# Kernel optimization log

Hardware: AMD Instinct MI355X
Metric: run time of the kernel (lower is better)

The kernel has to match this reference:

```python
import jax, jax.numpy as jnp
import numpy as np

EPS = 1e-13

def masked_softmax(scores, mask):
    # scores: [B, L1, L2], mask: [B, L2] binary float
    # ESIM-style: softmax(scores * mask) * mask, renormalized.
    m = mask[:, None, :]                      # [B, 1, L2]
    r = jax.nn.softmax(scores * m, axis=-1) * m
    return r / (r.sum(axis=-1, keepdims=True) + EPS)

def weighted_sum(attn, tensor, mask):
    # attn: [B, L1, L2], tensor: [B, L2, D], mask: [B, L1]
    return jnp.matmul(attn, tensor) * mask[:, :, None]

def setup_inputs() -> dict:
    key = jax.random.key(0)
    k1, k2, k3, k4 = jax.random.split(key, 4)
    B, Lp, Lh, D = 64, 512, 512, 600
    encoded_premise = jax.random.normal(k1, (B, Lp, D), dtype=jnp.float32)
    encoded_hypothesis = jax.random.normal(k2, (B, Lh, D), dtype=jnp.float32)
    # binary padding masks (1 = valid token)
    premise_mask = (jax.random.uniform(k3, (B, Lp)) > 0.15).astype(jnp.float32)
    hypothesis_mask = (jax.random.uniform(k4, (B, Lh)) > 0.15).astype(jnp.float32)
    return {"encoded_premise": encoded_premise, "premise_mask": premise_mask,
            "encoded_hypothesis": encoded_hypothesis, "hypothesis_mask": hypothesis_mask}

def reference(encoded_premise, premise_mask, encoded_hypothesis, hypothesis_mask):
    # shared cross-attention score matrix [B, Lp, Lh]
    attn = jnp.einsum('bpd,bhd->bph', encoded_premise, encoded_hypothesis)
    a_p = masked_softmax(attn, hypothesis_mask)                    # [B, Lp, Lh]
    a_h = masked_softmax(attn.transpose(0, 2, 1), premise_mask)    # [B, Lh, Lp]
    weighted_premise = weighted_sum(a_p, encoded_hypothesis, premise_mask)      # [B, Lp, D]
    weighted_hypothesis = weighted_sum(a_h, encoded_premise, hypothesis_mask)   # [B, Lh, D]
    return (weighted_premise, weighted_hypothesis)
```

## Files before the change

### kernel.cpp

```cpp
#include <hip/hip_runtime.h>
#include <hip/hip_bf16.h>

#define DEVB 64
#define LSEQ 512
#define DDIM 600

typedef short short8 __attribute__((ext_vector_type(8)));
typedef float f32x4 __attribute__((ext_vector_type(4)));
typedef _Float16 f16x8 __attribute__((ext_vector_type(8)));
typedef _Float16 f16x4 __attribute__((ext_vector_type(4)));

constexpr int LDP = 40;

__device__ __forceinline__ unsigned short f2bf(float x) {
    union { float f; unsigned u; } v; v.f = x;
    unsigned r = v.u + 0x7fffu + ((v.u >> 16) & 1u);
    return (unsigned short)(r >> 16);
}
__device__ __forceinline__ unsigned pk16(float a, float b) {
    union { _Float16 h[2]; unsigned u; } p;
    p.h[0] = (_Float16)a; p.h[1] = (_Float16)b;
    return p.u;
}
__device__ __forceinline__ f32x4 mfma16(short8 a, short8 b, f32x4 c) {
    return __builtin_amdgcn_mfma_f32_16x16x32_bf16(a, b, c, 0, 0, 0);
}
__device__ __forceinline__ f32x4 mfma16h(f16x8 a, f16x8 b, f32x4 c) {
    return __builtin_amdgcn_mfma_f32_16x16x32_f16(a, b, c, 0, 0, 0);
}

typedef const __attribute__((address_space(1))) unsigned int* as1_u32p;
typedef __attribute__((address_space(3))) unsigned int* as3_u32p;
__device__ __forceinline__ void gll16(const void* g, void* l) {
    __builtin_amdgcn_global_load_lds((as1_u32p)g, (as3_u32p)l, 16, 0, 0);
}

__global__ __launch_bounds__(256) void transcvt3(
    const float* __restrict__ P, const float* __restrict__ H,
    _Float16* __restrict__ pT, _Float16* __restrict__ hT)
{
    int blk = blockIdx.x;
    const float* X; _Float16* XT;
    const int half = DEVB * 40;
    if (blk < half) { X = P; XT = pT; }
    else { blk -= half; X = H; XT = hT; }

    int b   = blk / 40;
    int rem = blk % 40;
    int r0  = (rem / 5) << 6;
    int d0  = (rem % 5) << 7;
    const float* Xb = X + (size_t)b * LSEQ * DDIM;

    __shared__ unsigned T32[2][64 * 33];
    const int t  = threadIdx.x;
    const int rp = t >> 3;
    const int dc = (t & 7) << 3;

#pragma unroll
    for (int ht_ = 0; ht_ < 2; ++ht_) {
        int dd = d0 + (ht_ << 6) + dc;
        if (dd < DDIM) {
            const float* s0 = Xb + (size_t)(r0 + 2 * rp) * DDIM + dd;
            const float* s1 = s0 + DDIM;
            float4 a0 = *(const float4*)s0, a1 = *(const float4*)(s0 + 4);
            float4 b0 = *(const float4*)s1, b1 = *(const float4*)(s1 + 4);
            float xa[8] = {a0.x, a0.y, a0.z, a0.w, a1.x, a1.y, a1.z, a1.w};
            float xb[8] = {b0.x, b0.y, b0.z, b0.w, b1.x, b1.y, b1.z, b1.w};
#pragma unroll
            for (int j = 0; j < 8; ++j)
                T32[ht_][(dc + j) * 33 + rp] = pk16(xa[j], xb[j]);
        }
    }
    __syncthreads();

    const int dl = t >> 2;
    const int q  = t & 3;
#pragma unroll
    for (int ht_ = 0; ht_ < 2; ++ht_) {
        int d = d0 + (ht_ << 6) + dl;
        if (d < DDIM) {
            unsigned buf[8];
#pragma unroll
            for (int i = 0; i < 8; ++i)
                buf[i] = T32[ht_][dl * 33 + q * 8 + i];
            unsigned* dst = (unsigned*)(XT + ((size_t)b * DDIM + d) * LSEQ + r0) + q * 8;
            *(uint4*)(dst)     = *(uint4*)&buf[0];
            *(uint4*)(dst + 4) = *(uint4*)&buf[4];
        }
    }
}

__global__ __launch_bounds__(256) void attn_gemm(
    const float* __restrict__ P, const float* __restrict__ H,
    float* __restrict__ attn)
{
    const int bid = blockIdx.x;
    const int swz = (bid & 7) * 128 + (bid >> 3);
    const int b  = swz >> 4;
    const int pt = ((swz >> 2) & 3) << 7;
    const int ht = (swz & 3) << 7;
    const float* Pb = P + ((size_t)b * LSEQ + pt) * DDIM;
    const float* Hb = H + ((size_t)b * LSEQ + ht) * DDIM;
    float* Ab = attn + (size_t)b * LSEQ * LSEQ;

    __shared__ _Float16 Ah[2][128 * 32], Al[2][128 * 32], Bh[2][128 * 32];

    const int t    = threadIdx.x;
    const int lane = t & 63;
    const int wave = t >> 6;
    const int wm = (wave >> 1) << 6;
    const int wn = (wave & 1) << 6;
    const int fr = lane & 15;
    const int fq = lane >> 4;
    const int srow = t >> 2;
    const int sc8  = (t & 3) << 3;

    const int wchunk = (t & 3) ^ ((srow >> 1) & 3);
    const int woff   = srow * 32 + (wchunk << 3);
    const int rcoff  = ((fq ^ ((fr >> 1) & 3)) << 3);

    float4 pf[8];
    const float4 fz = {0.f, 0.f, 0.f, 0.f};
    auto issue = [&](int k0) {
        bool ok = (k0 + sc8) < DDIM;
#pragma unroll
        for (int r = 0; r < 2; ++r) {
            size_t base = (size_t)(srow + (r << 6)) * DDIM + k0 + sc8;
            if (ok) {
                pf[r * 4 + 0] = *(const float4*)(Pb + base);
                pf[r * 4 + 1] = *(const float4*)(Pb + base + 4);
                pf[r * 4 + 2] = *(const float4*)(Hb + base);
                pf[r * 4 + 3] = *(const float4*)(Hb + base + 4);
            } else {
                pf[r * 4 + 0] = fz; pf[r * 4 + 1] = fz;
                pf[r * 4 + 2] = fz; pf[r * 4 + 3] = fz;
            }
        }
    };
    auto wr = [&](int buf) {
#pragma unroll
        for (int r = 0; r < 2; ++r) {
            float4 a0 = pf[r * 4 + 0], a1 = pf[r * 4 + 1];
            float4 h0 = pf[r * 4 + 2], h1 = pf[r * 4 + 3];
            float af[8] = {a0.x, a0.y, a0.z, a0.w, a1.x, a1.y, a1.z, a1.w};
            float hf[8] = {h0.x, h0.y, h0.z, h0.w, h1.x, h1.y, h1.z, h1.w};
            f16x8 hi, lo, bh;
#pragma unroll
            for (int j = 0; j < 8; ++j) {
                hi[j] = (_Float16)af[j];
                lo[j] = (_Float16)(af[j] - (float)hi[j]);
                bh[j] = (_Float16)hf[j];
            }
            int off = woff + (r << 11);
            *(f16x8*)&Ah[buf][off] = hi;
            *(f16x8*)&Al[buf][off] = lo;
            *(f16x8*)&Bh[buf][off] = bh;
        }
    };

    issue(0);
    wr(0);
    issue(32);
    __syncthreads();

    f32x4 acc[4][4];
#pragma unroll
    for (int i = 0; i < 4; ++i)
#pragma unroll
        for (int j = 0; j < 4; ++j) acc[i][j] = (f32x4){0.f, 0.f, 0.f, 0.f};

    constexpr int NK = 19;
    int cur = 0;
    for (int it = 0; it < NK; ++it) {
        f16x8 ah[4], al[4], bh[4];
#pragma unroll
        for (int i = 0; i < 4; ++i) {
            int ra = (wm + (i << 4) + fr) * 32 + rcoff;
            int rb = (wn + (i << 4) + fr) * 32 + rcoff;
            ah[i] = *(const f16x8*)&Ah[cur][ra];
            al[i] = *(const f16x8*)&Al[cur][ra];
            bh[i] = *(const f16x8*)&Bh[cur][rb];
        }
        if (it + 1 < NK) {
            wr(cur ^ 1);
            if (it + 2 < NK) issue((it + 2) << 5);
        }
#pragma unroll
        for (int mi = 0; mi < 4; ++mi)
#pragma unroll
            for (int ni = 0; ni < 4; ++ni) {
                f32x4 c = acc[mi][ni];
                c = mfma16h(ah[mi], bh[ni], c);
                c = mfma16h(al[mi], bh[ni], c);
                acc[mi][ni] = c;
            }
        __syncthreads();
        cur ^= 1;
    }

#pragma unroll
    for (int mi = 0; mi < 4; ++mi)
#pragma unroll
        for (int ni = 0; ni < 4; ++ni)
#pragma unroll
            for (int j = 0; j < 4; ++j) {
                int p = pt + wm + (mi << 4) + (fq << 2) + j;
                int h = ht + wn + (ni << 4) + fr;
                Ab[(size_t)p * LSEQ + h] = acc[mi][ni][j];
            }
}

__global__ __launch_bounds__(256) void stats_w1(
    const float* __restrict__ attn, const float* __restrict__ hmask,
    const float* __restrict__ pmask,
    float* __restrict__ M1, float* __restrict__ R1,
    _Float16* __restrict__ W1,
    float* __restrict__ Mp, float* __restrict__ Tp, float* __restrict__ Sp)
{
    int b      = blockIdx.x >> 4;
    int stripe = blockIdx.x & 15;
    int lane   = threadIdx.x & 63;
    int wave   = threadIdx.x >> 6;
    const float* hm = hmask + (b << 9);
    const float* pm = pmask + (b << 9);

    float4 m0 = *(const float4*)(hm + (lane << 3));
    float4 m1 = *(const float4*)(hm + (lane << 3) + 4);
    float mk[8] = {m0.x, m0.y, m0.z, m0.w, m1.x, m1.y, m1.z, m1.w};

    float cM[8], cT[8], cS[8];
#pragma unroll
    for (int j = 0; j < 8; ++j) { cM[j] = -1e30f; cT[j] = 0.f; cS[j] = 0.f; }

    for (int i = 0; i < 8; ++i) {
        int row   = (stripe << 5) + (wave << 3) + i;
        int rowid = (b << 9) + row;
        const float* rp = attn + (size_t)rowid * LSEQ + (lane << 3);
        float4 s0 = *(const float4*)rp;
        float4 s1 = *(const float4*)(rp + 4);
        float s[8] = {s0.x, s0.y, s0.z, s0.w, s1.x, s1.y, s1.z, s1.w};

        float v[8];
#pragma unroll
        for (int j = 0; j < 8; ++j) v[j] = s[j] * mk[j];
        float mx = -1e30f;
#pragma unroll
        for (int j = 0; j < 8; ++j) mx = fmaxf(mx, v[j]);
#pragma unroll
        for (int off = 32; off; off >>= 1) mx = fmaxf(mx, __shfl_xor(mx, off));

        float e[8], T = 0.f, S = 0.f;
#pragma unroll
        for (int j = 0; j < 8; ++j) { e[j] = __expf(v[j] - mx); T += mk[j] * e[j]; S += e[j]; }
#pragma unroll
        for (int off = 32; off; off >>= 1) { T += __shfl_xor(T, off); S += __shfl_xor(S, off); }
        float R = 1.f / (T + 1e-13f * S);

        if (W1) {
            union { f16x8 v8; _Float16 h[8]; } wv;
#pragma unroll
            for (int j = 0; j < 8; ++j) wv.h[j] = (_Float16)(mk[j] * e[j] * R);
            *(f16x8*)(W1 + (size_t)rowid * LSEQ + (lane << 3)) = wv.v8;
        } else if (lane == 0) {
            M1[rowid] = mx; R1[rowid] = R;
        }

        float pmv = pm[row];
#pragma unroll
        for (int j = 0; j < 8; ++j) {
            float v2 = s[j] * pmv;
            float nm = fmaxf(cM[j], v2);
            float sc = __expf(cM[j] - nm);
            float e2 = __expf(v2 - nm);
            cT[j] = cT[j] * sc + pmv * e2;
            cS[j] = cS[j] * sc + e2;
            cM[j] = nm;
        }
    }

    __shared__ float LM[4][512], LT[4][512], LS[4][512];
#pragma unroll
    for (int j = 0; j < 8; ++j) {
        int c = (lane << 3) + j;
        LM[wave][c] = cM[j]; LT[wave][c] = cT[j]; LS[wave][c] = cS[j];
    }
    __syncthreads();

    size_t base = (size_t)((b << 4) + stripe) * 512;
    for (int cc = threadIdx.x; cc < 512; cc += 256) {
        float gm = fmaxf(fmaxf(LM[0][cc], LM[1][cc]), fmaxf(LM[2][cc], LM[3][cc]));
        float gT = 0.f, gS = 0.f;
#pragma unroll
        for (int w = 0; w < 4; ++w) {
            float sc = __expf(LM[w][cc] - gm);
            gT += LT[w][cc] * sc;
            gS += LS[w][cc] * sc;
        }
        Mp[base + cc] = gm; Tp[base + cc] = gT; Sp[base + cc] = gS;
    }
}

__global__ __launch_bounds__(256) void col_merge(
    const float* __restrict__ Mp, const float* __restrict__ Tp,
    const float* __restrict__ Sp, float* __restrict__ M2, float* __restrict__ R2)
{
    int b = blockIdx.x >> 1;
    int c = ((blockIdx.x & 1) << 8) + threadIdx.x;
    float gm = -1e30f, gT = 0.f, gS = 0.f;
#pragma unroll
    for (int st = 0; st < 16; ++st) {
        size_t idx = (size_t)((b << 4) + st) * 512 + c;
        float m = Mp[idx], tt = Tp[idx], ss = Sp[idx];
        float nm  = fmaxf(gm, m);
        float sc1 = __expf(gm - nm), sc2 = __expf(m - nm);
        gT = gT * sc1 + tt * sc2;
        gS = gS * sc1 + ss * sc2;
        gm = nm;
    }
    M2[(b << 9) + c] = gm;
    R2[(b << 9) + c] = 1.f / (gT + 1e-13f * gS);
}

__global__ __launch_bounds__(256) void w2gen3(
    const float* __restrict__ attn, const float* __restrict__ pmask,
    const float* __restrict__ Mp, const float* __restrict__ Tp,
    const float* __restrict__ Sp, _Float16* __restrict__ W2)
{
    int blk = blockIdx.x;
    int b  = blk >> 5;
    int p0 = ((blk >> 2) & 7) << 6;
    int h0 = (blk & 3) << 7;
    const float* Ab = attn + (size_t)b * LSEQ * LSEQ;
    const float* pm = pmask + (b << 9);

    __shared__ float sM[128], sR[128];
    __shared__ unsigned T32[128 * 33];
    const int t = threadIdx.x;
    if (t < 128) {
        float gm = -1e30f, gT = 0.f, gS = 0.f;
#pragma unroll
        for (int st = 0; st < 16; ++st) {
            size_t idx = (size_t)((b << 4) + st) * 512 + h0 + t;
            float m = Mp[idx], tt = Tp[idx], ss = Sp[idx];
            float nm  = fmaxf(gm, m);
            float sc1 = __expf(gm - nm), sc2 = __expf(m - nm);
            gT = gT * sc1 + tt * sc2;
            gS = gS * sc1 + ss * sc2;
            gm = nm;
        }
        sM[t] = gm;
        sR[t] = 1.f / (gT + 1e-13f * gS);
    }
    __syncthreads();

#pragma unroll
    for (int it = 0; it < 4; ++it) {
        int g  = t + (it << 8);
        int pp = g >> 5;
        int hc = (g & 31) << 2;
        const float* s0 = Ab + (size_t)(p0 + 2 * pp) * LSEQ + h0 + hc;
        float4 xa = *(const float4*)s0;
        float4 xb = *(const float4*)(s0 + LSEQ);
        float pa = pm[p0 + 2 * pp];
        float pb = pm[p0 + 2 * pp + 1];
        float a[4] = {xa.x, xa.y, xa.z, xa.w};
        float bb[4] = {xb.x, xb.y, xb.z, xb.w};
#pragma unroll
        for (int j = 0; j < 4; ++j) {
            float wa = (pa != 0.f) ? __expf(a[j]  - sM[hc + j]) * sR[hc + j] : 0.f;
            float wb = (pb != 0.f) ? __expf(bb[j] - sM[hc + j]) * sR[hc + j] : 0.f;
            T32[(hc + j) * 33 + pp] = pk16(wa, wb);
        }
    }
    __syncthreads();

    const int hl = t >> 1;
    const int q  = t & 1;
    unsigned buf[16];
#pragma unroll
    for (int i = 0; i < 16; ++i)
        buf[i] = T32[hl * 33 + q * 16 + i];
    unsigned* dst = (unsigned*)(W2 + ((size_t)(b << 9) + h0 + hl) * LSEQ + p0) + q * 16;
#pragma unroll
    for (int i = 0; i < 4; ++i)
        *(uint4*)(dst + 4 * i) = *(uint4*)&buf[4 * i];
}

__global__ __launch_bounds__(256) void gemm_gll(
    const _Float16* __restrict__ W, const _Float16* __restrict__ BT,
    const float* __restrict__ mask_m, float* __restrict__ out)
{
    const int bid = blockIdx.x;
    const int swz = (bid & 7) * 160 + (bid >> 3);
    const int b   = swz / 20;
    const int rem = swz % 20;
    const int m0  = (rem / 5) << 7;
    const int n0  = (rem % 5) << 7;
    const _Float16* Wb = W  + (size_t)b * LSEQ * LSEQ;
    const _Float16* Bb = BT + (size_t)b * DDIM * LSEQ;

    __shared__ _Float16 Wl[2][128 * 32];
    __shared__ _Float16 Bl[2][128 * 32];

    const int t    = threadIdx.x;
    const int lane = t & 63;
    const int wave = t >> 6;
    const int wm = (wave >> 1) << 6;
    const int wn = (wave & 1) << 6;
    const int fr = lane & 15;
    const int fq = lane >> 4;
    const int rcoff = ((fq ^ ((fr >> 1) & 3)) << 3);

    const int rowc0 = (wave << 5) + (lane >> 2);
    auto stage = [&](int buf, int k0) {
#pragma unroll
        for (int c = 0; c < 2; ++c) {
            int row = rowc0 + (c << 4);
            int lg  = (((lane & 3) ^ ((row >> 1) & 3)) << 3);
            int ldsoff = ((wave << 5) + (c << 4)) * 32;
            gll16(Wb + (size_t)(m0 + row) * LSEQ + k0 + lg, &Wl[buf][ldsoff]);
            gll16(Bb + (size_t)(n0 + row) * LSEQ + k0 + lg, &Bl[buf][ldsoff]);
        }
    };

    stage(0, 0);
    __syncthreads();

    f32x4 acc[4][4];
#pragma unroll
    for (int i = 0; i < 4; ++i)
#pragma unroll
        for (int j = 0; j < 4; ++j) acc[i][j] = (f32x4){0.f, 0.f, 0.f, 0.f};

    constexpr int NK = 16;
    for (int it = 0; it < NK; ++it) {
        int cur = it & 1;
        if (it + 1 < NK) stage(cur ^ 1, (it + 1) << 5);

        f16x8 af[4], bfr[4];
#pragma unroll
        for (int i = 0; i < 4; ++i) {
            af[i]  = *(const f16x8*)&Wl[cur][(wm + (i << 4) + fr) * 32 + rcoff];
            bfr[i] = *(const f16x8*)&Bl[cur][(wn + (i << 4) + fr) * 32 + rcoff];
        }
#pragma unroll
        for (int mi = 0; mi < 4; ++mi)
#pragma unroll
            for (int ni = 0; ni < 4; ++ni)
                acc[mi][ni] = mfma16h(af[mi], bfr[ni], acc[mi][ni]);
        __syncthreads();
    }

    const float* mmb = mask_m + (b << 9) + m0;
#pragma unroll
    for (int mi = 0; mi < 4; ++mi)
#pragma unroll
        for (int j = 0; j < 4; ++j) {
            int row = wm + (mi << 4) + (fq << 2) + j;
            float mm = mmb[row];
#pragma unroll
            for (int ni = 0; ni < 4; ++ni) {
                int d = n0 + wn + (ni << 4) + fr;
                if (d < DDIM)
                    out[((size_t)(b << 9) + m0 + row) * DDIM + d] = mm * acc[mi][ni][j];
            }
        }
}

template <int TRANSA>
__global__ __launch_bounds__(256) void wsum(
    const float* __restrict__ attn, const float* __restrict__ Bsrc,
    const float* __restrict__ mask_k, const float* __restrict__ mask_m,
    const float* __restrict__ Mst, const float* __restrict__ Rst,
    float* __restrict__ out)
{
    const int blk = blockIdx.x;
    const int b   = blk / 20;
    const int rem = blk % 20;
    const int m0  = (rem / 5) << 7;
    const int n0  = (rem % 5) << 7;

    const float* Ab  = attn + (size_t)b * LSEQ * LSEQ;
    const float* Bb  = Bsrc + (size_t)b * LSEQ * DDIM;
    const float* mkb = mask_k + (b << 9);

    __shared__ unsigned short Wl[128 * LDP];
    __shared__ unsigned short Bl[128 * LDP];
    __shared__ float Ml[128], Rl[128], Mm[128];

    const int t    = threadIdx.x;
    const int lane = t & 63;
    const int wave = t >> 6;
    const int wm = (wave >> 1) << 6;
    const int wn = (wave & 1) << 6;
    const int fr = lane & 15;
    const int fq = lane >> 4;

    if (t < 128) {
        Ml[t] = Mst[(b << 9) + m0 + t];
        Rl[t] = Rst[(b << 9) + m0 + t];
        Mm[t] = mask_m[(b << 9) + m0 + t];
    }
    __syncthreads();

    f32x4 acc[4][4];
#pragma unroll
    for (int i = 0; i < 4; ++i)
#pragma unroll
        for (int j = 0; j < 4; ++j) acc[i][j] = (f32x4){0.f, 0.f, 0.f, 0.f};

    for (int k0 = 0; k0 < LSEQ; k0 += 32) {
        if constexpr (TRANSA == 0) {
#pragma unroll
            for (int r = 0; r < 4; ++r) {
                int idx = t + (r << 8);
                int row = idx >> 3;
                int c4  = (idx & 7) << 2;
                float4 x  = *(const float4*)(Ab + (size_t)(m0 + row) * LSEQ + k0 + c4);
                float4 km = *(const float4*)(mkb + k0 + c4);
                float Mv = Ml[row], Rv = Rl[row];
                ushort4 w;
                w.x = (km.x != 0.f) ? f2bf(__expf(x.x - Mv) * Rv) : (unsigned short)0;
                w.y = (km.y != 0.f) ? f2bf(__expf(x.y - Mv) * Rv) : (unsigned short)0;
                w.z = (km.z != 0.f) ? f2bf(__expf(x.z - Mv) * Rv) : (unsigned short)0;
                w.w = (km.w != 0.f) ? f2bf(__expf(x.w - Mv) * Rv) : (unsigned short)0;
                *(ushort4*)&Wl[row * LDP + c4] = w;
            }
        } else {
#pragma unroll
            for (int r = 0; r < 4; ++r) {
                int mh = t & 127;
                int pq = (t >> 7) + (r << 1);
                float Mv = Ml[mh], Rv = Rl[mh];
                ushort4 w;
#pragma unroll
                for (int j = 0; j < 4; ++j) {
                    int k = k0 + (pq << 2) + j;
                    float x  = Ab[(size_t)k * LSEQ + m0 + mh];
                    float km = mkb[k];
                    ((unsigned short*)&w)[j] =
                        (km != 0.f) ? f2bf(__expf(x - Mv) * Rv) : (unsigned short)0;
                }
                *(ushort4*)&Wl[mh * LDP + (pq << 2)] = w;
            }
        }
#pragma unroll
        for (int r = 0; r < 4; ++r) {
            int d  = t & 127;
            int kq = (t >> 7) + (r << 1);
            bool valid = (n0 + d) < DDIM;
            ushort4 v;
#pragma unroll
            for (int j = 0; j < 4; ++j) {
                int k = k0 + (kq << 2) + j;
                float x = valid ? Bb[(size_t)k * DDIM + n0 + d] : 0.f;
                ((unsigned short*)&v)[j] = f2bf(x);
            }
            *(ushort4*)&Bl[d * LDP + (kq << 2)] = v;
        }
        __syncthreads();

        short8 af[4], bfr[4];
#pragma unroll
        for (int i = 0; i < 4; ++i) {
            af[i]  = *(const short8*)&Wl[(wm + (i << 4) + fr) * LDP + (fq << 3)];
            bfr[i] = *(const short8*)&Bl[(wn + (i << 4) + fr) * LDP + (fq << 3)];
        }
#pragma unroll
        for (int mi = 0; mi < 4; ++mi)
#pragma unroll
            for (int ni = 0; ni < 4; ++ni)
                acc[mi][ni] = mfma16(af[mi], bfr[ni], acc[mi][ni]);
        __syncthreads();
    }

#pragma unroll
    for (int mi = 0; mi < 4; ++mi)
#pragma unroll
        for (int j = 0; j < 4; ++j) {
            int row = wm + (mi << 4) + (fq << 2) + j;
            float mm = Mm[row];
#pragma unroll
            for (int ni = 0; ni < 4; ++ni) {
                int d = n0 + wn + (ni << 4) + fr;
                if (d < DDIM)
                    out[((size_t)(b << 9) + m0 + row) * DDIM + d] = mm * acc[mi][ni][j];
            }
        }
}

extern "C" void kernel_launch(void* const* d_in, const int* in_sizes, int n_in,
                              void* d_out, int out_size, void* d_ws, size_t ws_size,
                              hipStream_t stream)
{
    const float* P  = (const float*)d_in[0];
    const float* pm = (const float*)d_in[1];
    const float* H  = (const float*)d_in[2];
    const float* hm = (const float*)d_in[3];
    float* out = (float*)d_out;
    char* o  = (char*)d_out;
    char* ws = (char*)d_ws;

    const size_t E = (size_t)DEVB * LSEQ * DDIM;

    _Float16* hT = (_Float16*)(o + 78643200);
    _Float16* W1 = (_Float16*)(o + 117964800);

    const size_t fast_need = 146276352;

    if (ws_size >= fast_need) {
        float*     attn = (float*)ws;
        _Float16*  pT   = (_Float16*)(ws + 67108864);
        _Float16*  W2   = (_Float16*)(ws + 67108864 + 39321600);
        float*     Mp   = (float*)(ws + 139984896);
        float*     Tp   = Mp + (size_t)DEVB * 16 * 512;
        float*     Sp   = Tp + (size_t)DEVB * 16 * 512;

        transcvt3<<<DEVB * 80, 256, 0, stream>>>(P, H, pT, hT);
        attn_gemm<<<DEVB * 16, 256, 0, stream>>>(P, H, attn);
        stats_w1<<<DEVB * 16, 256, 0, stream>>>(attn, hm, pm, nullptr, nullptr,
                                                W1, Mp, Tp, Sp);
        w2gen3<<<DEVB * 32, 256, 0, stream>>>(attn, pm, Mp, Tp, Sp, W2);
        gemm_gll<<<DEVB * 20, 256, 0, stream>>>(W1, hT, pm, out);
        gemm_gll<<<DEVB * 20, 256, 0, stream>>>(W2, pT, hm, out + E);
    } else {
        float* attn = (float*)ws;
        float* Mp   = (float*)(ws + 67108864);
        float* Tp   = Mp + (size_t)DEVB * 16 * 512;
        float* Sp   = Tp + (size_t)DEVB * 16 * 512;
        float* M1   = Sp + (size_t)DEVB * 16 * 512;
        float* R1   = M1 + DEVB * LSEQ;
        float* M2   = R1 + DEVB * LSEQ;
        float* R2   = M2 + DEVB * LSEQ;

        attn_gemm<<<DEVB * 16, 256, 0, stream>>>(P, H, attn);
        stats_w1<<<DEVB * 16, 256, 0, stream>>>(attn, hm, pm, M1, R1, nullptr,
                                                Mp, Tp, Sp);
        col_merge<<<DEVB * 2, 256, 0, stream>>>(Mp, Tp, Sp, M2, R2);
        wsum<0><<<DEVB * 20, 256, 0, stream>>>(attn, H, hm, pm, M1, R1, out);
        wsum<1><<<DEVB * 20, 256, 0, stream>>>(attn, P, pm, hm, M2, R2, out + E);
    }
}
```

Baseline: 301.3 us.

## Precompute padded fp16 H in transpose kernel and stage it via global_load_lds

The transpose/convert kernel now also writes a row-major fp16 copy of H with K padded to 608 into scratch space in the output buffer. The attention GEMM reads this half-size copy and loads its B tile directly into LDS with global_load_lds, instead of loading fp32 H through registers and converting it. This cuts the GEMM's global read traffic for H and its conversion work, at the cost of an extra fp16 write in the prepass. The fallback path now runs the prepass just to produce this copy.

```diff
diff --git a/kernel.cpp b/kernel.cpp
--- a/kernel.cpp
+++ b/kernel.cpp
@@ -4,6 +4,7 @@
 #define DEVB 64
 #define LSEQ 512
 #define DDIM 600
+#define KPAD 608
 
 typedef short short8 __attribute__((ext_vector_type(8)));
 typedef float f32x4 __attribute__((ext_vector_type(4)));
@@ -37,13 +38,14 @@
 
 __global__ __launch_bounds__(256) void transcvt3(
     const float* __restrict__ P, const float* __restrict__ H,
-    _Float16* __restrict__ pT, _Float16* __restrict__ hT)
+    _Float16* __restrict__ pT, _Float16* __restrict__ hT,
+    _Float16* __restrict__ Hhi)
 {
     int blk = blockIdx.x;
-    const float* X; _Float16* XT;
+    const float* X; _Float16* XT; _Float16* RM;
     const int half = DEVB * 40;
-    if (blk < half) { X = P; XT = pT; }
-    else { blk -= half; X = H; XT = hT; }
+    if (blk < half) { X = P; XT = pT; RM = nullptr; }
+    else { blk -= half; X = H; XT = hT; RM = Hhi; }
 
     int b   = blk / 40;
     int rem = blk % 40;
@@ -69,29 +71,46 @@
 #pragma unroll
             for (int j = 0; j < 8; ++j)
                 T32[ht_][(dc + j) * 33 + rp] = pk16(xa[j], xb[j]);
-        }
+            if (RM) {
+                f16x8 ha, hb;
+#pragma unroll
+                for (int j = 0; j < 8; ++j) {
+                    ha[j] = (_Float16)xa[j];
+                    hb[j] = (_Float16)xb[j];
+                }
+                _Float16* rm0 = RM + ((size_t)b * LSEQ + r0 + 2 * rp) * KPAD + dd;
+                *(f16x8*)rm0          = ha;
+                *(f16x8*)(rm0 + KPAD) = hb;
+            }
+        }
+    }
+    if (RM && d0 == 512 && t < 64) {
+        const f16x8 z = {0, 0, 0, 0, 0, 0, 0, 0};
+        *(f16x8*)(RM + ((size_t)b * LSEQ + r0 + t) * KPAD + DDIM) = z;
     }
     __syncthreads();
 
-    const int dl = t >> 2;
-    const int q  = t & 3;
-#pragma unroll
-    for (int ht_ = 0; ht_ < 2; ++ht_) {
-        int d = d0 + (ht_ << 6) + dl;
-        if (d < DDIM) {
-            unsigned buf[8];
-#pragma unroll
-            for (int i = 0; i < 8; ++i)
-                buf[i] = T32[ht_][dl * 33 + q * 8 + i];
-            unsigned* dst = (unsigned*)(XT + ((size_t)b * DDIM + d) * LSEQ + r0) + q * 8;
-            *(uint4*)(dst)     = *(uint4*)&buf[0];
-            *(uint4*)(dst + 4) = *(uint4*)&buf[4];
+    if (XT) {
+        const int dl = t >> 2;
+        const int q  = t & 3;
+#pragma unroll
+        for (int ht_ = 0; ht_ < 2; ++ht_) {
+            int d = d0 + (ht_ << 6) + dl;
+            if (d < DDIM) {
+                unsigned buf[8];
+#pragma unroll
+                for (int i = 0; i < 8; ++i)
+                    buf[i] = T32[ht_][dl * 33 + q * 8 + i];
+                unsigned* dst = (unsigned*)(XT + ((size_t)b * DDIM + d) * LSEQ + r0) + q * 8;
+                *(uint4*)(dst)     = *(uint4*)&buf[0];
+                *(uint4*)(dst + 4) = *(uint4*)&buf[4];
+            }
         }
     }
 }
 
 __global__ __launch_bounds__(256) void attn_gemm(
-    const float* __restrict__ P, const float* __restrict__ H,
+    const float* __restrict__ P, const _Float16* __restrict__ Hhi,
     float* __restrict__ attn)
 {
     const int bid = blockIdx.x;
@@ -99,8 +118,8 @@
     const int b  = swz >> 4;
     const int pt = ((swz >> 2) & 3) << 7;
     const int ht = (swz & 3) << 7;
-    const float* Pb = P + ((size_t)b * LSEQ + pt) * DDIM;
-    const float* Hb = H + ((size_t)b * LSEQ + ht) * DDIM;
+    const float*    Pb = P   + ((size_t)b * LSEQ + pt) * DDIM;
+    const _Float16* Hb = Hhi + ((size_t)b * LSEQ + ht) * KPAD;
     float* Ab = attn + (size_t)b * LSEQ * LSEQ;
 
     __shared__ _Float16 Ah[2][128 * 32], Al[2][128 * 32], Bh[2][128 * 32];
@@ -119,7 +138,18 @@
     const int woff   = srow * 32 + (wchunk << 3);
     const int rcoff  = ((fq ^ ((fr >> 1) & 3)) << 3);
 
-    float4 pf[8];
+    const int rowc0 = (wave << 5) + (lane >> 2);
+    auto bstage = [&](int buf, int k0) {
+#pragma unroll
+        for (int c = 0; c < 2; ++c) {
+            int row = rowc0 + (c << 4);
+            int lg  = (((lane & 3) ^ ((row >> 1) & 3)) << 3);
+            int ldsoff = ((wave << 5) + (c << 4)) * 32;
+            gll16(Hb + (size_t)row * KPAD + k0 + lg, &Bh[buf][ldsoff]);
+        }
+    };
+
+    float4 pf[4];
     const float4 fz = {0.f, 0.f, 0.f, 0.f};
     auto issue = [&](int k0) {
         bool ok = (k0 + sc8) < DDIM;
@@ -127,37 +157,31 @@
         for (int r = 0; r < 2; ++r) {
             size_t base = (size_t)(srow + (r << 6)) * DDIM + k0 + sc8;
             if (ok) {
-                pf[r * 4 + 0] = *(const float4*)(Pb + base);
-                pf[r * 4 + 1] = *(const float4*)(Pb + base + 4);
-                pf[r * 4 + 2] = *(const float4*)(Hb + base);
-                pf[r * 4 + 3] = *(const float4*)(Hb + base + 4);
+                pf[r * 2 + 0] = *(const float4*)(Pb + base);
+                pf[r * 2 + 1] = *(const float4*)(Pb + base + 4);
             } else {
-                pf[r * 4 + 0] = fz; pf[r * 4 + 1] = fz;
-                pf[r * 4 + 2] = fz; pf[r * 4 + 3] = fz;
+                pf[r * 2 + 0] = fz; pf[r * 2 + 1] = fz;
             }
         }
     };
     auto wr = [&](int buf) {
 #pragma unroll
         for (int r = 0; r < 2; ++r) {
-            float4 a0 = pf[r * 4 + 0], a1 = pf[r * 4 + 1];
-            float4 h0 = pf[r * 4 + 2], h1 = pf[r * 4 + 3];
+            float4 a0 = pf[r * 2 + 0], a1 = pf[r * 2 + 1];
             float af[8] = {a0.x, a0.y, a0.z, a0.w, a1.x, a1.y, a1.z, a1.w};
-            float hf[8] = {h0.x, h0.y, h0.z, h0.w, h1.x, h1.y, h1.z, h1.w};
-            f16x8 hi, lo, bh;
+            f16x8 hi, lo;
 #pragma unroll
             for (int j = 0; j < 8; ++j) {
                 hi[j] = (_Float16)af[j];
                 lo[j] = (_Float16)(af[j] - (float)hi[j]);
-                bh[j] = (_Float16)hf[j];
             }
             int off = woff + (r << 11);
             *(f16x8*)&Ah[buf][off] = hi;
             *(f16x8*)&Al[buf][off] = lo;
-            *(f16x8*)&Bh[buf][off] = bh;
         }
     };
 
+    bstage(0, 0);
     issue(0);
     wr(0);
     issue(32);
@@ -183,6 +207,7 @@
         }
         if (it + 1 < NK) {
             wr(cur ^ 1);
+            bstage(cur ^ 1, (it + 1) << 5);
             if (it + 2 < NK) issue((it + 2) << 5);
         }
 #pragma unroll
@@ -603,8 +628,9 @@
 
     const size_t E = (size_t)DEVB * LSEQ * DDIM;
 
-    _Float16* hT = (_Float16*)(o + 78643200);
-    _Float16* W1 = (_Float16*)(o + 117964800);
+    _Float16* Hhi = (_Float16*)o;
+    _Float16* hT  = (_Float16*)(o + 78643200);
+    _Float16* W1  = (_Float16*)(o + 117964800);
 
     const size_t fast_need = 146276352;
 
@@ -616,8 +642,8 @@
         float*     Tp   = Mp + (size_t)DEVB * 16 * 512;
         float*     Sp   = Tp + (size_t)DEVB * 16 * 512;
 
-        transcvt3<<<DEVB * 80, 256, 0, stream>>>(P, H, pT, hT);
-        attn_gemm<<<DEVB * 16, 256, 0, stream>>>(P, H, attn);
+        transcvt3<<<DEVB * 80, 256, 0, stream>>>(P, H, pT, hT, Hhi);
+        attn_gemm<<<DEVB * 16, 256, 0, stream>>>(P, Hhi, attn);
         stats_w1<<<DEVB * 16, 256, 0, stream>>>(attn, hm, pm, nullptr, nullptr,
                                                 W1, Mp, Tp, Sp);
         w2gen3<<<DEVB * 32, 256, 0, stream>>>(attn, pm, Mp, Tp, Sp, W2);
@@ -633,7 +659,8 @@
         float* M2   = R1 + DEVB * LSEQ;
         float* R2   = M2 + DEVB * LSEQ;
 
-        attn_gemm<<<DEVB * 16, 256, 0, stream>>>(P, H, attn);
+        transcvt3<<<DEVB * 80, 256, 0, stream>>>(P, H, nullptr, nullptr, Hhi);
+        attn_gemm<<<DEVB * 16, 256, 0, stream>>>(P, Hhi, attn);
         stats_w1<<<DEVB * 16, 256, 0, stream>>>(attn, hm, pm, M1, R1, nullptr,
                                                 Mp, Tp, Sp);
         col_merge<<<DEVB * 2, 256, 0, stream>>>(Mp, Tp, Sp, M2, R2);
```

Result: slower. 337.3 us (+12.0%).
